# Optimization experiments

Measured on AMD Instinct MI355X. Metric: run time of the kernel, lower is better.

Reference implementation:

```python
import jax, jax.numpy as jnp
import numpy as np

D_MODEL = 512
NHEAD = 8


def setup_inputs() -> dict:
    key = jax.random.key(0)
    ks = jax.random.split(key, 8)
    d = D_MODEL
    low_feats = jax.random.normal(ks[0], (1, d, 32, 32), dtype=jnp.float32)
    guide_feats = jax.random.normal(ks[1], (1, d, 128, 128), dtype=jnp.float32)
    s = 1.0 / np.sqrt(d)
    Wq = jax.random.normal(ks[2], (d, d), dtype=jnp.float32) * s
    Wk = jax.random.normal(ks[3], (d, d), dtype=jnp.float32) * s
    Wv = jax.random.normal(ks[4], (d, d), dtype=jnp.float32) * s
    Wm = jax.random.normal(ks[5], (d, d), dtype=jnp.float32) * s
    gamma = jnp.ones((d,), dtype=jnp.float32)
    beta = jnp.zeros((d,), dtype=jnp.float32)
    return {"low_feats": low_feats, "guide_feats": guide_feats, "Wq": Wq,
            "Wk": Wk, "Wv": Wv, "Wm": Wm, "gamma": gamma, "beta": beta}


def _gather_windows(feat_hw, H, W):
    # feat_hw: [b, h, w, nhead, dim]. For each guide pixel (Y,X), nearest low
    # pixel is (Y*h//H, X*w//W) (PyTorch 'nearest'); gather its 3x3 neighborhood
    # with replicate padding (index clamping). Window order = ky*3+kx, matching
    # F.unfold channel layout. Returns [b, H*W, 9, nhead, dim].
    b, h, w, nh, dm = feat_hw.shape
    offs = jnp.array([-1, 0, 1])
    y0 = jnp.arange(H) * h // H                      # [H]
    x0 = jnp.arange(W) * w // W                      # [W]
    ys = jnp.clip(y0[:, None] + offs, 0, h - 1)      # [H,3] (ky)
    xs = jnp.clip(x0[:, None] + offs, 0, w - 1)      # [W,3] (kx)
    # -> [b, H, W, 3(ky), 3(kx), nhead, dim]
    g = feat_hw[:, ys[:, None, :, None], xs[None, :, None, :]]
    return g.reshape(b, H * W, 9, nh, dm)


def reference(low_feats, guide_feats, Wq, Wk, Wv, Wm, gamma, beta):
    b, d, H, W = guide_feats.shape
    _, _, h, w = low_feats.shape
    nh = NHEAD
    dm = d // nh
    g = guide_feats.transpose(0, 2, 3, 1).reshape(b, H * W, d)
    l = low_feats.transpose(0, 2, 3, 1).reshape(b, h * w, d)
    q = (g @ Wq.T).reshape(b, H * W, nh, dm)                 # [b,N,h,d]
    K = (l @ Wk.T).reshape(b, h, w, nh, dm)
    V = (l @ Wv.T).reshape(b, h, w, nh, dm)
    key = _gather_windows(K, H, W)                           # [b,N,9,h,d]
    val = _gather_windows(V, H, W)
    scale = 1.0 / jnp.sqrt(jnp.asarray(dm, dtype=q.dtype))
    # (q/sqrt(dm)) @ (k/sqrt(dm)) * sqrt(dm) == q@k / sqrt(dm)
    score = jnp.einsum('bnhd,bnkhd->bnhk', q, key) * scale
    attn = jax.nn.softmax(score, axis=-1)
    msg = jnp.einsum('bnhk,bnkhd->bnhd', attn, val).reshape(b, H * W, d)
    msg = msg @ Wm.T
    # LayerNorm(d_model), eps=1e-5
    mu = jnp.mean(msg, axis=-1, keepdims=True)
    var = jnp.mean((msg - mu) ** 2, axis=-1, keepdims=True)
    msg = (msg - mu) * jax.lax.rsqrt(var + 1e-5) * gamma + beta
    return msg.transpose(0, 2, 1).reshape(b, d, H, W)
```

## Files before the change

### kernel.cpp

```cpp
#include <hip/hip_runtime.h>
#include <hip/hip_bf16.h>
#include <stdint.h>

#define NQ 16384
#define NL 1024

typedef __bf16 bf16_t;
typedef __bf16 bf16x8 __attribute__((ext_vector_type(8)));
typedef __bf16 bf16x4 __attribute__((ext_vector_type(4)));
typedef float f32x4 __attribute__((ext_vector_type(4)));

__device__ __forceinline__ void gload_lds16(const void* g, void* l) {
  __builtin_amdgcn_global_load_lds(
      (const __attribute__((address_space(1))) uint32_t*)g,
      (__attribute__((address_space(3))) uint32_t*)l, 16, 0, 0);
}

__global__ __launch_bounds__(256) void cvt_transpose_all(const float* __restrict__ guide,
                                                         const float* __restrict__ low,
                                                         bf16_t* __restrict__ Gbf,
                                                         bf16_t* __restrict__ Lbf) {
  __shared__ float tl[32][33];
  const float* src;
  bf16_t* dst;
  int ncols, n0;
  if (blockIdx.x < 512) { src = guide; dst = Gbf; ncols = NQ; n0 = blockIdx.x * 32; }
  else                  { src = low;   dst = Lbf; ncols = NL; n0 = (blockIdx.x - 512) * 32; }
  const int c0 = blockIdx.y * 32;
  const int t = threadIdx.x, c = t & 31, r = t >> 5;
#pragma unroll
  for (int it = 0; it < 4; ++it) {
    int rr = r + it * 8;
    tl[rr][c] = src[(size_t)(c0 + rr) * ncols + n0 + c];
  }
  __syncthreads();
#pragma unroll
  for (int it = 0; it < 4; ++it) {
    int rr = r + it * 8;
    dst[(size_t)(n0 + rr) * 512 + c0 + c] = (bf16_t)tl[c][rr];
  }
}

__global__ __launch_bounds__(256) void cvt_w(const float* __restrict__ s0, const float* __restrict__ s1,
                                             const float* __restrict__ s2, const float* __restrict__ s3,
                                             bf16_t* __restrict__ d0, bf16_t* __restrict__ d1,
                                             bf16_t* __restrict__ d2, bf16_t* __restrict__ d3) {
  const float* s;
  bf16_t* d;
  switch (blockIdx.y) {
    case 0: s = s0; d = d0; break;
    case 1: s = s1; d = d1; break;
    case 2: s = s2; d = d2; break;
    default: s = s3; d = d3; break;
  }
  const int i = (blockIdx.x * 256 + threadIdx.x) * 4;
  float4 v = *(const float4*)(s + i);
  bf16x4 o = {(bf16_t)v.x, (bf16_t)v.y, (bf16_t)v.z, (bf16_t)v.w};
  *(bf16x4*)(d + i) = o;
}

__global__ __launch_bounds__(256) void gemm_qkv(const bf16_t* __restrict__ G,
                                                const bf16_t* __restrict__ Wq,
                                                bf16_t* __restrict__ Qo,
                                                const bf16_t* __restrict__ L,
                                                const bf16_t* __restrict__ Wkv,
                                                bf16_t* __restrict__ KVo) {
  __shared__ __align__(16) bf16_t As[128 * 64];
  __shared__ __align__(16) bf16_t Bs[128 * 64];
  const bf16_t *A, *B;
  bf16_t* C;
  int N, bm, bn;
  const int bid = blockIdx.x;
  if (bid < 512) { A = G; B = Wq; C = Qo; N = 512; bm = (bid >> 2) * 128; bn = (bid & 3) * 128; }
  else { int id = bid - 512; A = L; B = Wkv; C = KVo; N = 1024; bm = (id >> 3) * 128; bn = (id & 7) * 128; }
  const int t = threadIdx.x;
  const int lane = t & 63;
  const int wave = t >> 6;
  const int wr = (wave >> 1) * 64;
  const int wc = (wave & 1) * 64;
  const int r0 = t >> 3;
  const int c0 = (t & 7) * 8;
  f32x4 acc[4][4] = {};
  for (int k0 = 0; k0 < 512; k0 += 64) {
#pragma unroll
    for (int it = 0; it < 4; ++it) {
      const int r = r0 + it * 32;
      gload_lds16(A + (size_t)(bm + r) * 512 + k0 + c0, &As[r * 64 + c0]);
      gload_lds16(B + (size_t)(bn + r) * 512 + k0 + c0, &Bs[r * 64 + c0]);
    }
    __syncthreads();
#pragma unroll
    for (int kk = 0; kk < 2; ++kk) {
      bf16x8 af[4], bfv[4];
#pragma unroll
      for (int i = 0; i < 4; ++i)
        af[i] = *(const bf16x8*)&As[(wr + i * 16 + (lane & 15)) * 64 + kk * 32 + (lane >> 4) * 8];
#pragma unroll
      for (int i = 0; i < 4; ++i)
        bfv[i] = *(const bf16x8*)&Bs[(wc + i * 16 + (lane & 15)) * 64 + kk * 32 + (lane >> 4) * 8];
#pragma unroll
      for (int i = 0; i < 4; ++i)
#pragma unroll
        for (int j = 0; j < 4; ++j)
          acc[i][j] = __builtin_amdgcn_mfma_f32_16x16x32_bf16(af[i], bfv[j], acc[i][j], 0, 0, 0);
    }
    __syncthreads();
  }
  const int crow = bm + wr + ((lane >> 4) * 4);
  const int ccol = bn + wc + (lane & 15);
#pragma unroll
  for (int i = 0; i < 4; ++i)
#pragma unroll
    for (int j = 0; j < 4; ++j) {
      const int row = crow + i * 16;
      const int col = ccol + j * 16;
#pragma unroll
      for (int v = 0; v < 4; ++v)
        C[(size_t)(row + v) * N + col] = (bf16_t)acc[i][j][v];
    }
}

__global__ __launch_bounds__(128) void attn_win(const bf16_t* __restrict__ Q,
                                                const bf16_t* __restrict__ KV,
                                                bf16_t* __restrict__ Msg) {
  __shared__ __align__(16) bf16_t Kl[9 * 512];
  __shared__ __align__(16) bf16_t Vl[9 * 512];
  const int t = threadIdx.x;
  const int lane = t & 63;
  const int wave = t >> 6;
  const int tile = blockIdx.x;
  const int ty = tile >> 5, tx = tile & 31;
  for (int kk = wave; kk < 9; kk += 2) {
    int ky = kk / 3, kx = kk - ky * 3;
    int yy = min(max(ty - 1 + ky, 0), 31);
    int xx = min(max(tx - 1 + kx, 0), 31);
    size_t p = (size_t)(yy * 32 + xx) * 1024;
    int dst = kk * 512 + (lane & 7) * 64 + (lane >> 3) * 8;
    *(bf16x8*)&Kl[dst] = *(const bf16x8*)&KV[p + lane * 8];
    *(bf16x8*)&Vl[dst] = *(const bf16x8*)&KV[p + 512 + lane * 8];
  }
  __syncthreads();
  const int pl = t >> 3, h = t & 7;
  const int y = ty * 4 + (pl >> 2), x = tx * 4 + (pl & 3);
  const size_t n = (size_t)y * 128 + x;
  const bf16_t* qrow = Q + n * 512 + h * 64;
  float s[9] = {};
#pragma unroll
  for (int i8 = 0; i8 < 8; ++i8) {
    bf16x8 q8 = *(const bf16x8*)(qrow + i8 * 8);
#pragma unroll
    for (int k = 0; k < 9; ++k) {
      bf16x8 k8 = *(const bf16x8*)&Kl[k * 512 + i8 * 64 + h * 8];
#pragma unroll
      for (int e = 0; e < 8; ++e) s[k] += (float)q8[e] * (float)k8[e];
    }
  }
  float mx = s[0];
#pragma unroll
  for (int k = 1; k < 9; ++k) mx = fmaxf(mx, s[k]);
  float sum = 0.f;
#pragma unroll
  for (int k = 0; k < 9; ++k) {
    s[k] = __expf((s[k] - mx) * 0.125f);
    sum += s[k];
  }
  const float inv = 1.0f / sum;
#pragma unroll
  for (int k = 0; k < 9; ++k) s[k] *= inv;
  bf16_t* orow = Msg + n * 512 + h * 64;
#pragma unroll
  for (int i8 = 0; i8 < 8; ++i8) {
    float accv[8] = {};
#pragma unroll
    for (int k = 0; k < 9; ++k) {
      bf16x8 v8 = *(const bf16x8*)&Vl[k * 512 + i8 * 64 + h * 8];
#pragma unroll
      for (int e = 0; e < 8; ++e) accv[e] += s[k] * (float)v8[e];
    }
    bf16x8 o;
#pragma unroll
    for (int e = 0; e < 8; ++e) o[e] = (bf16_t)accv[e];
    *(bf16x8*)&orow[i8 * 8] = o;
  }
}

__global__ __launch_bounds__(512) void gemm_ln_out(const bf16_t* __restrict__ A,
                                                   const bf16_t* __restrict__ B,
                                                   const float* __restrict__ gamma,
                                                   const float* __restrict__ beta,
                                                   float* __restrict__ out) {
  __shared__ __align__(16) char smem[64 * 513 * 4];
  __shared__ float2 part[64][4];
  __shared__ float2 st[64];
  bf16_t* As = (bf16_t*)smem;
  bf16_t* Bs = (bf16_t*)(smem + 8192);
  float* Cl = (float*)smem;
  const int t = threadIdx.x;
  const int lane = t & 63;
  const int wave = t >> 6;
  const int wr = (wave >> 2) * 32;
  const int wc = (wave & 3) * 128;
  const int bm = blockIdx.x * 64;
  const int sr = t >> 3;
  const int sc = (t & 7) * 8;
  f32x4 acc[2][8] = {};
  for (int k0 = 0; k0 < 512; k0 += 64) {
    gload_lds16(A + (size_t)(bm + sr) * 512 + k0 + sc, &As[sr * 64 + sc]);
#pragma unroll
    for (int it = 0; it < 8; ++it) {
      const int r = sr + it * 64;
      gload_lds16(B + (size_t)r * 512 + k0 + sc, &Bs[r * 64 + sc]);
    }
    __syncthreads();
#pragma unroll
    for (int kk = 0; kk < 2; ++kk) {
      bf16x8 af[2], bfv[8];
#pragma unroll
      for (int i = 0; i < 2; ++i)
        af[i] = *(const bf16x8*)&As[(wr + i * 16 + (lane & 15)) * 64 + kk * 32 + (lane >> 4) * 8];
#pragma unroll
      for (int j = 0; j < 8; ++j)
        bfv[j] = *(const bf16x8*)&Bs[(wc + j * 16 + (lane & 15)) * 64 + kk * 32 + (lane >> 4) * 8];
#pragma unroll
      for (int i = 0; i < 2; ++i)
#pragma unroll
        for (int j = 0; j < 8; ++j)
          acc[i][j] = __builtin_amdgcn_mfma_f32_16x16x32_bf16(af[i], bfv[j], acc[i][j], 0, 0, 0);
    }
    __syncthreads();
  }
#pragma unroll
  for (int i = 0; i < 2; ++i)
#pragma unroll
    for (int j = 0; j < 8; ++j) {
      const int row = wr + i * 16 + (lane >> 4) * 4;
      const int col = wc + j * 16 + (lane & 15);
#pragma unroll
      for (int v = 0; v < 4; ++v) Cl[(row + v) * 513 + col] = acc[i][j][v];
    }
#pragma unroll
  for (int i = 0; i < 2; ++i)
#pragma unroll
    for (int v = 0; v < 4; ++v) {
      float s = 0.f, s2 = 0.f;
#pragma unroll
      for (int j = 0; j < 8; ++j) {
        float x = acc[i][j][v];
        s += x;
        s2 += x * x;
      }
#pragma unroll
      for (int m = 1; m < 16; m <<= 1) {
        s += __shfl_xor(s, m, 64);
        s2 += __shfl_xor(s2, m, 64);
      }
      if ((lane & 15) == 0) {
        const int row = wr + i * 16 + (lane >> 4) * 4 + v;
        part[row][wave & 3] = make_float2(s, s2);
      }
    }
  __syncthreads();
  if (t < 64) {
    float2 p0 = part[t][0], p1 = part[t][1], p2 = part[t][2], p3 = part[t][3];
    float s = p0.x + p1.x + p2.x + p3.x;
    float s2 = p0.y + p1.y + p2.y + p3.y;
    float mu = s * (1.f / 512.f);
    float var = s2 * (1.f / 512.f) - mu * mu;
    st[t] = make_float2(mu, rsqrtf(var + 1e-5f));
  }
  __syncthreads();
  const int n = t & 63;
  const int j0 = t >> 6;
  const float2 ms = st[n];
#pragma unroll 8
  for (int jj = 0; jj < 64; ++jj) {
    const int j = j0 * 64 + jj;
    const float g = gamma[j], b = beta[j];
    const float x = Cl[n * 513 + j];
    out[(size_t)j * NQ + bm + n] = (x - ms.x) * ms.y * g + b;
  }
}

extern "C" void kernel_launch(void* const* d_in, const int* in_sizes, int n_in,
                              void* d_out, int out_size, void* d_ws, size_t ws_size,
                              hipStream_t stream) {
  const float* low = (const float*)d_in[0];
  const float* guide = (const float*)d_in[1];
  const float* Wq = (const float*)d_in[2];
  const float* Wk = (const float*)d_in[3];
  const float* Wv = (const float*)d_in[4];
  const float* Wm = (const float*)d_in[5];
  const float* gamma = (const float*)d_in[6];
  const float* beta = (const float*)d_in[7];
  float* out = (float*)d_out;

  char* w = (char*)d_ws;
  bf16_t* Gbf = (bf16_t*)w; w += (size_t)NQ * 512 * 2;
  bf16_t* Lbf = (bf16_t*)w; w += (size_t)NL * 512 * 2;
  bf16_t* Wqb = (bf16_t*)w; w += (size_t)512 * 512 * 2;
  bf16_t* Wkvb = (bf16_t*)w; w += (size_t)1024 * 512 * 2;
  bf16_t* Wmb = (bf16_t*)w; w += (size_t)512 * 512 * 2;
  bf16_t* Qbf = (bf16_t*)w; w += (size_t)NQ * 512 * 2;
  bf16_t* KVbf = (bf16_t*)w; w += (size_t)NL * 1024 * 2;
  bf16_t* Msg = (bf16_t*)w; w += (size_t)NQ * 512 * 2;

  cvt_transpose_all<<<dim3(544, 16), 256, 0, stream>>>(guide, low, Gbf, Lbf);
  cvt_w<<<dim3(256, 4), 256, 0, stream>>>(Wq, Wk, Wv, Wm, Wqb, Wkvb, Wkvb + (size_t)512 * 512, Wmb);
  gemm_qkv<<<dim3(576), 256, 0, stream>>>(Gbf, Wqb, Qbf, Lbf, Wkvb, KVbf);
  attn_win<<<dim3(1024), 128, 0, stream>>>(Qbf, KVbf, Msg);
  gemm_ln_out<<<dim3(NQ / 64), 512, 0, stream>>>(Msg, Wmb, gamma, beta, out);
}
```

Baseline: 174.5 us.

## Double-buffer LDS tiles in both GEMMs and merge conversion kernels

Adds a two-stage LDS double buffer to the QKV and output GEMMs, so the next K-tile's global-to-LDS loads are issued before computing on the current tile. The weight conversion is also folded into the input transpose kernel, removing one launch, and the bf16 weights are packed into a single buffer. This costs more LDS per block (about 147KB in the output GEMM), which could limit occupancy, and relies on the barrier to wait on the async loads.

Result: faster. 168.9 us (-3.2%).

```diff
diff --git a/kernel.cpp b/kernel.cpp
--- a/kernel.cpp
+++ b/kernel.cpp
@@ -16,18 +16,37 @@
       (__attribute__((address_space(3))) uint32_t*)l, 16, 0, 0);
 }
 
-__global__ __launch_bounds__(256) void cvt_transpose_all(const float* __restrict__ guide,
-                                                         const float* __restrict__ low,
-                                                         bf16_t* __restrict__ Gbf,
-                                                         bf16_t* __restrict__ Lbf) {
+__global__ __launch_bounds__(256) void cvt_all(const float* __restrict__ guide,
+                                               const float* __restrict__ low,
+                                               const float* __restrict__ Wq,
+                                               const float* __restrict__ Wk,
+                                               const float* __restrict__ Wv,
+                                               const float* __restrict__ Wm,
+                                               bf16_t* __restrict__ Gbf,
+                                               bf16_t* __restrict__ Lbf,
+                                               bf16_t* __restrict__ Wall) {
+  const int bx = blockIdx.x, by = blockIdx.y, t = threadIdx.x;
+  if (bx >= 544) {
+    const int idx = (((bx - 544) * 16 + by) * 256 + t) * 4;
+    const float* s;
+    int off;
+    if (idx < 262144)      { s = Wq; off = idx; }
+    else if (idx < 524288) { s = Wk; off = idx - 262144; }
+    else if (idx < 786432) { s = Wv; off = idx - 524288; }
+    else                   { s = Wm; off = idx - 786432; }
+    float4 v = *(const float4*)(s + off);
+    bf16x4 o = {(bf16_t)v.x, (bf16_t)v.y, (bf16_t)v.z, (bf16_t)v.w};
+    *(bf16x4*)(Wall + idx) = o;
+    return;
+  }
   __shared__ float tl[32][33];
   const float* src;
   bf16_t* dst;
   int ncols, n0;
-  if (blockIdx.x < 512) { src = guide; dst = Gbf; ncols = NQ; n0 = blockIdx.x * 32; }
-  else                  { src = low;   dst = Lbf; ncols = NL; n0 = (blockIdx.x - 512) * 32; }
-  const int c0 = blockIdx.y * 32;
-  const int t = threadIdx.x, c = t & 31, r = t >> 5;
+  if (bx < 512) { src = guide; dst = Gbf; ncols = NQ; n0 = bx * 32; }
+  else          { src = low;   dst = Lbf; ncols = NL; n0 = (bx - 512) * 32; }
+  const int c0 = by * 32;
+  const int c = t & 31, r = t >> 5;
 #pragma unroll
   for (int it = 0; it < 4; ++it) {
     int rr = r + it * 8;
@@ -41,37 +60,19 @@
   }
 }
 
-__global__ __launch_bounds__(256) void cvt_w(const float* __restrict__ s0, const float* __restrict__ s1,
-                                             const float* __restrict__ s2, const float* __restrict__ s3,
-                                             bf16_t* __restrict__ d0, bf16_t* __restrict__ d1,
-                                             bf16_t* __restrict__ d2, bf16_t* __restrict__ d3) {
-  const float* s;
-  bf16_t* d;
-  switch (blockIdx.y) {
-    case 0: s = s0; d = d0; break;
-    case 1: s = s1; d = d1; break;
-    case 2: s = s2; d = d2; break;
-    default: s = s3; d = d3; break;
-  }
-  const int i = (blockIdx.x * 256 + threadIdx.x) * 4;
-  float4 v = *(const float4*)(s + i);
-  bf16x4 o = {(bf16_t)v.x, (bf16_t)v.y, (bf16_t)v.z, (bf16_t)v.w};
-  *(bf16x4*)(d + i) = o;
-}
-
 __global__ __launch_bounds__(256) void gemm_qkv(const bf16_t* __restrict__ G,
-                                                const bf16_t* __restrict__ Wq,
+                                                const bf16_t* __restrict__ Wqb,
                                                 bf16_t* __restrict__ Qo,
                                                 const bf16_t* __restrict__ L,
                                                 const bf16_t* __restrict__ Wkv,
                                                 bf16_t* __restrict__ KVo) {
-  __shared__ __align__(16) bf16_t As[128 * 64];
-  __shared__ __align__(16) bf16_t Bs[128 * 64];
+  __shared__ __align__(16) bf16_t As[2][128 * 64];
+  __shared__ __align__(16) bf16_t Bs[2][128 * 64];
   const bf16_t *A, *B;
   bf16_t* C;
   int N, bm, bn;
   const int bid = blockIdx.x;
-  if (bid < 512) { A = G; B = Wq; C = Qo; N = 512; bm = (bid >> 2) * 128; bn = (bid & 3) * 128; }
+  if (bid < 512) { A = G; B = Wqb; C = Qo; N = 512; bm = (bid >> 2) * 128; bn = (bid & 3) * 128; }
   else { int id = bid - 512; A = L; B = Wkv; C = KVo; N = 1024; bm = (id >> 3) * 128; bn = (id & 7) * 128; }
   const int t = threadIdx.x;
   const int lane = t & 63;
@@ -80,24 +81,38 @@
   const int wc = (wave & 1) * 64;
   const int r0 = t >> 3;
   const int c0 = (t & 7) * 8;
+  const int fr = lane & 15;
+  const int fk = (lane >> 4) * 8;
+#pragma unroll
+  for (int it = 0; it < 4; ++it) {
+    const int r = r0 + it * 32;
+    gload_lds16(A + (size_t)(bm + r) * 512 + c0, &As[0][r * 64 + c0]);
+    gload_lds16(B + (size_t)(bn + r) * 512 + c0, &Bs[0][r * 64 + c0]);
+  }
   f32x4 acc[4][4] = {};
-  for (int k0 = 0; k0 < 512; k0 += 64) {
-#pragma unroll
-    for (int it = 0; it < 4; ++it) {
-      const int r = r0 + it * 32;
-      gload_lds16(A + (size_t)(bm + r) * 512 + k0 + c0, &As[r * 64 + c0]);
-      gload_lds16(B + (size_t)(bn + r) * 512 + k0 + c0, &Bs[r * 64 + c0]);
-    }
-    __syncthreads();
+  __syncthreads();
+#pragma unroll 2
+  for (int kt = 0; kt < 8; ++kt) {
+    const int cur = kt & 1;
+    if (kt < 7) {
+      const int k0 = (kt + 1) * 64;
+#pragma unroll
+      for (int it = 0; it < 4; ++it) {
+        const int r = r0 + it * 32;
+        gload_lds16(A + (size_t)(bm + r) * 512 + k0 + c0, &As[cur ^ 1][r * 64 + c0]);
+        gload_lds16(B + (size_t)(bn + r) * 512 + k0 + c0, &Bs[cur ^ 1][r * 64 + c0]);
+      }
+    }
+    __builtin_amdgcn_sched_barrier(0);
 #pragma unroll
     for (int kk = 0; kk < 2; ++kk) {
       bf16x8 af[4], bfv[4];
 #pragma unroll
       for (int i = 0; i < 4; ++i)
-        af[i] = *(const bf16x8*)&As[(wr + i * 16 + (lane & 15)) * 64 + kk * 32 + (lane >> 4) * 8];
+        af[i] = *(const bf16x8*)&As[cur][(wr + i * 16 + fr) * 64 + kk * 32 + fk];
 #pragma unroll
       for (int i = 0; i < 4; ++i)
-        bfv[i] = *(const bf16x8*)&Bs[(wc + i * 16 + (lane & 15)) * 64 + kk * 32 + (lane >> 4) * 8];
+        bfv[i] = *(const bf16x8*)&Bs[cur][(wc + i * 16 + fr) * 64 + kk * 32 + fk];
 #pragma unroll
       for (int i = 0; i < 4; ++i)
 #pragma unroll
@@ -107,7 +122,7 @@
     __syncthreads();
   }
   const int crow = bm + wr + ((lane >> 4) * 4);
-  const int ccol = bn + wc + (lane & 15);
+  const int ccol = bn + wc + fr;
 #pragma unroll
   for (int i = 0; i < 4; ++i)
 #pragma unroll
@@ -189,12 +204,14 @@
                                                    const float* __restrict__ gamma,
                                                    const float* __restrict__ beta,
                                                    float* __restrict__ out) {
-  __shared__ __align__(16) char smem[64 * 513 * 4];
+  __shared__ __align__(16) char smem[147456];
   __shared__ float2 part[64][4];
   __shared__ float2 st[64];
-  bf16_t* As = (bf16_t*)smem;
-  bf16_t* Bs = (bf16_t*)(smem + 8192);
-  float* Cl = (float*)smem;
+  bf16_t* const As0 = (bf16_t*)smem;
+  bf16_t* const As1 = (bf16_t*)(smem + 8192);
+  bf16_t* const Bs0 = (bf16_t*)(smem + 16384);
+  bf16_t* const Bs1 = (bf16_t*)(smem + 81920);
+  float* const Cl = (float*)smem;
   const int t = threadIdx.x;
   const int lane = t & 63;
   const int wave = t >> 6;
@@ -203,24 +220,41 @@
   const int bm = blockIdx.x * 64;
   const int sr = t >> 3;
   const int sc = (t & 7) * 8;
+  const int fr = lane & 15;
+  const int fk = (lane >> 4) * 8;
+  gload_lds16(A + (size_t)(bm + sr) * 512 + sc, &As0[sr * 64 + sc]);
+#pragma unroll
+  for (int it = 0; it < 8; ++it) {
+    const int r = sr + it * 64;
+    gload_lds16(B + (size_t)r * 512 + sc, &Bs0[r * 64 + sc]);
+  }
   f32x4 acc[2][8] = {};
-  for (int k0 = 0; k0 < 512; k0 += 64) {
-    gload_lds16(A + (size_t)(bm + sr) * 512 + k0 + sc, &As[sr * 64 + sc]);
-#pragma unroll
-    for (int it = 0; it < 8; ++it) {
-      const int r = sr + it * 64;
-      gload_lds16(B + (size_t)r * 512 + k0 + sc, &Bs[r * 64 + sc]);
-    }
-    __syncthreads();
+  __syncthreads();
+#pragma unroll 2
+  for (int kt = 0; kt < 8; ++kt) {
+    bf16_t* const Asc = (kt & 1) ? As1 : As0;
+    bf16_t* const Bsc = (kt & 1) ? Bs1 : Bs0;
+    bf16_t* const Asn = (kt & 1) ? As0 : As1;
+    bf16_t* const Bsn = (kt & 1) ? Bs0 : Bs1;
+    if (kt < 7) {
+      const int k0 = (kt + 1) * 64;
+      gload_lds16(A + (size_t)(bm + sr) * 512 + k0 + sc, &Asn[sr * 64 + sc]);
+#pragma unroll
+      for (int it = 0; it < 8; ++it) {
+        const int r = sr + it * 64;
+        gload_lds16(B + (size_t)r * 512 + k0 + sc, &Bsn[r * 64 + sc]);
+      }
+    }
+    __builtin_amdgcn_sched_barrier(0);
 #pragma unroll
     for (int kk = 0; kk < 2; ++kk) {
       bf16x8 af[2], bfv[8];
 #pragma unroll
       for (int i = 0; i < 2; ++i)
-        af[i] = *(const bf16x8*)&As[(wr + i * 16 + (lane & 15)) * 64 + kk * 32 + (lane >> 4) * 8];
+        af[i] = *(const bf16x8*)&Asc[(wr + i * 16 + fr) * 64 + kk * 32 + fk];
 #pragma unroll
       for (int j = 0; j < 8; ++j)
-        bfv[j] = *(const bf16x8*)&Bs[(wc + j * 16 + (lane & 15)) * 64 + kk * 32 + (lane >> 4) * 8];
+        bfv[j] = *(const bf16x8*)&Bsc[(wc + j * 16 + fr) * 64 + kk * 32 + fk];
 #pragma unroll
       for (int i = 0; i < 2; ++i)
 #pragma unroll
@@ -234,7 +268,7 @@
 #pragma unroll
     for (int j = 0; j < 8; ++j) {
       const int row = wr + i * 16 + (lane >> 4) * 4;
-      const int col = wc + j * 16 + (lane & 15);
+      const int col = wc + j * 16 + fr;
 #pragma unroll
       for (int v = 0; v < 4; ++v) Cl[(row + v) * 513 + col] = acc[i][j][v];
     }
@@ -295,18 +329,15 @@
   float* out = (float*)d_out;
 
   char* w = (char*)d_ws;
-  bf16_t* Gbf = (bf16_t*)w; w += (size_t)NQ * 512 * 2;
-  bf16_t* Lbf = (bf16_t*)w; w += (size_t)NL * 512 * 2;
-  bf16_t* Wqb = (bf16_t*)w; w += (size_t)512 * 512 * 2;
-  bf16_t* Wkvb = (bf16_t*)w; w += (size_t)1024 * 512 * 2;
-  bf16_t* Wmb = (bf16_t*)w; w += (size_t)512 * 512 * 2;
-  bf16_t* Qbf = (bf16_t*)w; w += (size_t)NQ * 512 * 2;
+  bf16_t* Gbf = (bf16_t*)w;  w += (size_t)NQ * 512 * 2;
+  bf16_t* Lbf = (bf16_t*)w;  w += (size_t)NL * 512 * 2;
+  bf16_t* Wall = (bf16_t*)w; w += (size_t)4 * 512 * 512 * 2;
+  bf16_t* Qbf = (bf16_t*)w;  w += (size_t)NQ * 512 * 2;
   bf16_t* KVbf = (bf16_t*)w; w += (size_t)NL * 1024 * 2;
-  bf16_t* Msg = (bf16_t*)w; w += (size_t)NQ * 512 * 2;
-
-  cvt_transpose_all<<<dim3(544, 16), 256, 0, stream>>>(guide, low, Gbf, Lbf);
-  cvt_w<<<dim3(256, 4), 256, 0, stream>>>(Wq, Wk, Wv, Wm, Wqb, Wkvb, Wkvb + (size_t)512 * 512, Wmb);
-  gemm_qkv<<<dim3(576), 256, 0, stream>>>(Gbf, Wqb, Qbf, Lbf, Wkvb, KVbf);
+  bf16_t* Msg = (bf16_t*)w;  w += (size_t)NQ * 512 * 2;
+
+  cvt_all<<<dim3(608, 16), 256, 0, stream>>>(guide, low, Wq, Wk, Wv, Wm, Gbf, Lbf, Wall);
+  gemm_qkv<<<dim3(576), 256, 0, stream>>>(Gbf, Wall, Qbf, Lbf, Wall + 262144, KVbf);
   attn_win<<<dim3(1024), 128, 0, stream>>>(Qbf, KVbf, Msg);
-  gemm_ln_out<<<dim3(NQ / 64), 512, 0, stream>>>(Msg, Wmb, gamma, beta, out);
-}
+  gemm_ln_out<<<dim3(NQ / 64), 512, 0, stream>>>(Msg, Wall + 786432, gamma, beta, out);
+}
```
